# Performance work log

Measured on AMD Instinct MI355X. Metric: run time of the kernel, lower is better.

The kernel has to match this reference:

```python
import jax, jax.numpy as jnp
import numpy as np

D = 1024
H = 16
DH = D // H
F = 4096
B, S = 4, 2048
EPS = 1e-5


def _ln(x, g, b):
    m = jnp.mean(x, axis=-1, keepdims=True)
    v = jnp.var(x, axis=-1, keepdims=True)
    return (x - m) * jax.lax.rsqrt(v + EPS) * g + b


def setup_inputs() -> dict:
    key = jax.random.key(0)
    ks = jax.random.split(key, 16)
    s = 0.02
    return {
        "x": jax.random.normal(ks[0], (B, S, D), jnp.float32),
        "key_padding_mask": jnp.zeros((B, S), jnp.bool_),
        "Wq": jax.random.normal(ks[1], (D, D), jnp.float32) * s,
        "bq": jnp.zeros((D,), jnp.float32),
        "Wk": jax.random.normal(ks[2], (D, D), jnp.float32) * s,
        "bk": jnp.zeros((D,), jnp.float32),
        "Wv": jax.random.normal(ks[3], (D, D), jnp.float32) * s,
        "bv": jnp.zeros((D,), jnp.float32),
        "Wo": jax.random.normal(ks[4], (D, D), jnp.float32) * s,
        "bo": jnp.zeros((D,), jnp.float32),
        "W1": jax.random.normal(ks[5], (F, D), jnp.float32) * s,
        "b1": jnp.zeros((F,), jnp.float32),
        "W2": jax.random.normal(ks[6], (D, F), jnp.float32) * s,
        "b2": jnp.zeros((D,), jnp.float32),
        "ln1_g": jnp.ones((D,), jnp.float32),
        "ln1_b": jnp.zeros((D,), jnp.float32),
        "ln2_g": jnp.ones((D,), jnp.float32),
        "ln2_b": jnp.zeros((D,), jnp.float32),
    }


def _attn(x, kpm, Wq, bq, Wk, bk, Wv, bv, Wo, bo):
    b, s, d = x.shape
    scaling = DH ** (-0.5)
    q = (x @ Wq.T + bq) * scaling
    k = x @ Wk.T + bk
    v = x @ Wv.T + bv
    q = q.reshape(b, s, H, DH)
    k = k.reshape(b, s, H, DH)
    v = v.reshape(b, s, H, DH)
    # [b,h,q,k]
    scores = jnp.einsum("bqhd,bkhd->bhqk", q, k)
    scores = jnp.where(kpm[:, None, None, :], -jnp.inf, scores)
    p = jax.nn.softmax(scores.astype(jnp.float32), axis=-1).astype(q.dtype)
    out = jnp.einsum("bhqk,bkhd->bqhd", p, v).reshape(b, s, d)
    return out @ Wo.T + bo


def reference(x, key_padding_mask, Wq, bq, Wk, bk, Wv, bv, Wo, bo,
              W1, b1, W2, b2, ln1_g, ln1_b, ln2_g, ln2_b):
    # post-LN (normalize_before=False), dropout in eval mode (identity)
    x = _ln(x + _attn(x, key_padding_mask, Wq, bq, Wk, bk, Wv, bv, Wo, bo), ln1_g, ln1_b)
    h = jax.nn.gelu(x @ W1.T + b1, approximate=False)
    x = _ln(x + (h @ W2.T + b2), ln2_g, ln2_b)
    return x
```

## Files before the change

kernel.cpp:

```cpp
#include <hip/hip_runtime.h>
#include <hip/hip_bf16.h>
#include <math.h>

typedef short bf16x8 __attribute__((ext_vector_type(8)));
typedef float f32x4 __attribute__((ext_vector_type(4)));

__device__ __forceinline__ unsigned short f2bfu(float f) {
    __hip_bfloat16 h = __float2bfloat16(f);
    return __builtin_bit_cast(unsigned short, h);
}

__device__ __forceinline__ float fexp2(float x) {
    float r;
    asm("v_exp_f32 %0, %1" : "=v"(r) : "v"(x));
    return r;
}

__device__ __forceinline__ unsigned cvtpk_bf16(float lo, float hi) {
    unsigned r;
    asm("v_cvt_pk_bf16_f32 %0, %1, %2" : "=v"(r) : "v"(lo), "v"(hi));
    return r;
}

__device__ __forceinline__ float gelu_fast(float x) {
    const float x2 = x * x;
    const float z = x * (0.7978845608f + 0.0356774081f * x2);
    const float e = fexp2(z * 2.88539008f);
    const float r = __builtin_amdgcn_rcpf(e + 1.0f);
    return x * (1.0f - r);
}

__device__ __forceinline__ void gload_lds16(const void* gsrc, void* ldst) {
    __builtin_amdgcn_global_load_lds((const __attribute__((address_space(1))) void*)gsrc,
                                     (__attribute__((address_space(3))) void*)ldst,
                                     16, 0, 0);
}

#define MFMA __builtin_amdgcn_mfma_f32_16x16x32_bf16

__global__ __launch_bounds__(256)
void cvt_bf16_kernel(const float4* __restrict__ in, ushort4* __restrict__ out, int n4) {
    int i = blockIdx.x * 256 + threadIdx.x;
    if (i >= n4) return;
    float4 v = in[i];
    ushort4 o;
    o.x = f2bfu(v.x); o.y = f2bfu(v.y); o.z = f2bfu(v.z); o.w = f2bfu(v.w);
    out[i] = o;
}

enum { EPI_QKV = 0, EPI_RESF32 = 2, EPI_GELU = 3, EPI_RESBF16 = 5 };

template<int EPI>
__global__ __launch_bounds__(256, 3)
void gemm_bt(const __hip_bfloat16* __restrict__ A,
             const __hip_bfloat16* __restrict__ W,
             const float* __restrict__ bias,
             const void* __restrict__ resv,
             float scale,
             void* __restrict__ outp, void* __restrict__ outp2, void* __restrict__ outp3,
             int M, int N, int K)
{
    __shared__ __hip_bfloat16 As[3][128 * 32];
    __shared__ __hip_bfloat16 Ws[3][128 * 32];
    const int tid = threadIdx.x;
    const int lane = tid & 63;
    const int wid = tid >> 6;
    const int wr = wid >> 1, wc = wid & 1;
    const int g = lane >> 4, lr = lane & 15;
    const int row0 = blockIdx.x * 128;
    const int col0 = blockIdx.y * 128;

    f32x4 acc[4][4];
    const f32x4 zero = {0.f, 0.f, 0.f, 0.f};
#pragma unroll
    for (int m = 0; m < 4; ++m)
#pragma unroll
        for (int n = 0; n < 4; ++n) acc[m][n] = zero;

    const int c0 = tid, c1 = tid + 256;
    const int ar0 = c0 >> 2, ac0 = (c0 & 3) * 8;
    const int ar1 = c1 >> 2, ac1 = (c1 & 3) * 8;
    const __hip_bfloat16* Arow0 = A + (size_t)(row0 + ar0) * K + ac0;
    const __hip_bfloat16* Arow1 = A + (size_t)(row0 + ar1) * K + ac1;
    const __hip_bfloat16* Wrow0 = W + (size_t)(col0 + ar0) * K + ac0;
    const __hip_bfloat16* Wrow1 = W + (size_t)(col0 + ar1) * K + ac1;

    auto stage = [&](int bi, int k0) {
        gload_lds16(Arow0 + k0, (char*)As[bi] + c0 * 16);
        gload_lds16(Arow1 + k0, (char*)As[bi] + c1 * 16);
        gload_lds16(Wrow0 + k0, (char*)Ws[bi] + c0 * 16);
        gload_lds16(Wrow1 + k0, (char*)Ws[bi] + c1 * 16);
    };

    const int NT = K >> 5;
    stage(0, 0);
    stage(1, 32);
    asm volatile("s_waitcnt vmcnt(4)" ::: "memory");
    __builtin_amdgcn_s_barrier();
    __builtin_amdgcn_sched_barrier(0);

    int cur = 0, stg = 2;
    int kpre = 64;
    for (int t = 0; t < NT; ++t) {
        if (t + 2 < NT) stage(stg, kpre);

        bf16x8 af[4], wf[4];
#pragma unroll
        for (int m = 0; m < 4; ++m)
            af[m] = *(const bf16x8*)(As[cur] + (wr * 64 + m * 16 + lr) * 32 + g * 8);
#pragma unroll
        for (int n = 0; n < 4; ++n)
            wf[n] = *(const bf16x8*)(Ws[cur] + (wc * 64 + n * 16 + lr) * 32 + g * 8);
#pragma unroll
        for (int m = 0; m < 4; ++m)
#pragma unroll
            for (int n = 0; n < 4; ++n)
                acc[m][n] = MFMA(af[m], wf[n], acc[m][n], 0, 0, 0);

        if (t + 1 < NT) {
            if (t + 2 < NT) asm volatile("s_waitcnt vmcnt(4)" ::: "memory");
            else            asm volatile("s_waitcnt vmcnt(0)" ::: "memory");
            __builtin_amdgcn_s_barrier();
            __builtin_amdgcn_sched_barrier(0);
        }
        cur = (cur == 2) ? 0 : cur + 1;
        stg = (stg == 2) ? 0 : stg + 1;
        kpre += 32;
    }

#pragma unroll
    for (int n = 0; n < 4; ++n) {
        const int cc = col0 + wc * 64 + n * 16 + lr;
        const float bv = bias[cc];
#pragma unroll
        for (int m = 0; m < 4; ++m) {
            const int rbase = row0 + wr * 64 + m * 16 + g * 4;
            if (EPI == EPI_QKV) {
                const int seg = col0 >> 10;
                if (seg == 2) {
                    ushort4 u;
                    u.x = f2bfu(acc[m][n][0] + bv);
                    u.y = f2bfu(acc[m][n][1] + bv);
                    u.z = f2bfu(acc[m][n][2] + bv);
                    u.w = f2bfu(acc[m][n][3] + bv);
                    const int cc2 = cc - 2048;
                    const int h_ = cc2 >> 6, dh = cc2 & 63;
                    const int bb = rbase >> 11;
                    const int s = rbase & 2047;
                    *(ushort4*)((__hip_bfloat16*)outp3 +
                                (((size_t)bb * 16 + h_) * 64 + dh) * 2048 + s) = u;
                } else {
                    const float sc = (seg == 0) ? scale : 1.0f;
                    __hip_bfloat16* dst = (seg == 0) ? (__hip_bfloat16*)outp
                                                     : (__hip_bfloat16*)outp2;
                    const int ccl = cc & 1023;
#pragma unroll
                    for (int r = 0; r < 4; ++r)
                        dst[(size_t)(rbase + r) * 1024 + ccl] =
                            __float2bfloat16((acc[m][n][r] + bv) * sc);
                }
            } else {
#pragma unroll
                for (int r = 0; r < 4; ++r) {
                    const size_t idx = (size_t)(rbase + r) * N + cc;
                    float v = acc[m][n][r] + bv;
                    if (EPI == EPI_RESF32) {
                        ((float*)outp)[idx] = v + ((const float*)resv)[idx];
                    } else if (EPI == EPI_RESBF16) {
                        ((float*)outp)[idx] = v +
                            __bfloat162float(((const __hip_bfloat16*)resv)[idx]);
                    } else if (EPI == EPI_GELU) {
                        ((__hip_bfloat16*)outp)[idx] = __float2bfloat16(gelu_fast(v));
                    }
                }
            }
        }
    }
}

__global__ __launch_bounds__(256, 2)
void attn_flash2(const __hip_bfloat16* __restrict__ Q,
                 const __hip_bfloat16* __restrict__ K,
                 const __hip_bfloat16* __restrict__ VT,
                 const unsigned char* __restrict__ kpm,
                 __hip_bfloat16* __restrict__ O)
{
    __shared__ __hip_bfloat16 Ks[2][64 * 64];
    __shared__ __hip_bfloat16 VTs[2][64 * 64];
    __shared__ __hip_bfloat16 Plds[4][64 * 64];

    const int tid = threadIdx.x;
    const int lane = tid & 63;
    const int w = tid >> 6;
    const int g = lane >> 4, lr = lane & 15;

    const int orig = blockIdx.y * 8 + blockIdx.x;
    const int nl = (orig & 7) * 64 + (orig >> 3);
    const int qb = nl & 7;
    const int bh = nl >> 3;

    const int b = bh >> 4, h = bh & 15;
    const int q0 = qb * 256 + w * 64;
    const size_t tokbase = (size_t)b * 2048;
    const __hip_bfloat16* VTbh = VT + (size_t)bh * 64 * 2048;

    unsigned tmask = 0;
#pragma unroll
    for (int i = 0; i < 8; ++i) {
        const unsigned mv = *(const unsigned*)(kpm + tokbase + i * 256 + lane * 4);
        const unsigned long long bal = __ballot((int)(mv != 0u));
#pragma unroll
        for (int j = 0; j < 4; ++j)
            if ((bal >> (16 * j)) & 0xFFFFull) tmask |= (1u << (i * 4 + j));
    }

    bf16x8 qf[4][2];
#pragma unroll
    for (int qn = 0; qn < 4; ++qn)
#pragma unroll
        for (int f = 0; f < 2; ++f)
            qf[qn][f] = *(const bf16x8*)(Q + (tokbase + q0 + qn * 16 + lr) * 1024 +
                                         h * 64 + f * 32 + g * 8);

    f32x4 o[4][4];
    const f32x4 zero = {0.f, 0.f, 0.f, 0.f};
#pragma unroll
    for (int qa = 0; qa < 4; ++qa)
#pragma unroll
        for (int nd = 0; nd < 4; ++nd) o[qa][nd] = zero;
    float m_run[4], l_part[4];
#pragma unroll
    for (int qn = 0; qn < 4; ++qn) { m_run[qn] = -1e30f; l_part[qn] = 0.f; }

    __hip_bfloat16* Pw = Plds[w];
    const int rowl = lane >> 3;
    const int blkp = lane & 7;

    auto stage = [&](int bufi, int kv0) {
#pragma unroll
        for (int iss = 0; iss < 2; ++iss) {
            const int row = w * 16 + iss * 8 + rowl;
            const int sblk = blkp ^ (row & 7);
            gload_lds16(K + (tokbase + kv0 + row) * 1024 + h * 64 + sblk * 8,
                        (char*)&Ks[bufi][(w * 16 + iss * 8) * 64] + lane * 16);
            gload_lds16(VTbh + (size_t)row * 2048 + kv0 + sblk * 8,
                        (char*)&VTs[bufi][(w * 16 + iss * 8) * 64] + lane * 16);
        }
    };

    stage(0, 0);
    __syncthreads();
    int buf = 0;

    for (int t = 0; t < 32; ++t) {
        const int kv0 = t * 64;
        if (t < 31) stage(buf ^ 1, kv0 + 64);

        f32x4 st[4][4];
        __builtin_amdgcn_s_setprio(1);
#pragma unroll
        for (int km = 0; km < 4; ++km) {
            bf16x8 kf[2];
#pragma unroll
            for (int f = 0; f < 2; ++f)
                kf[f] = *(const bf16x8*)(&Ks[buf][(km * 16 + lr) * 64 +
                                                  (((f * 4 + g) ^ (lr & 7)) * 8)]);
#pragma unroll
            for (int qn = 0; qn < 4; ++qn) {
                st[km][qn] = MFMA(kf[0], qf[qn][0], zero, 0, 0, 0);
                st[km][qn] = MFMA(kf[1], qf[qn][1], st[km][qn], 0, 0, 0);
            }
        }
        __builtin_amdgcn_s_setprio(0);

        if (tmask & (1u << t)) {
            const float NEG = -1e30f;
#pragma unroll
            for (int km = 0; km < 4; ++km) {
                const unsigned mu = *(const unsigned*)(kpm + tokbase + kv0 + km * 16 + g * 4);
#pragma unroll
                for (int r = 0; r < 4; ++r) {
                    if ((mu >> (8 * r)) & 0xFFu) {
#pragma unroll
                        for (int qn = 0; qn < 4; ++qn) st[km][qn][r] = NEG;
                    }
                }
            }
        }

        float pm[4];
#pragma unroll
        for (int qn = 0; qn < 4; ++qn) {
            float a0 = fmaxf(fmaxf(st[0][qn][0], st[0][qn][1]), fmaxf(st[0][qn][2], st[0][qn][3]));
            float a1 = fmaxf(fmaxf(st[1][qn][0], st[1][qn][1]), fmaxf(st[1][qn][2], st[1][qn][3]));
            float a2 = fmaxf(fmaxf(st[2][qn][0], st[2][qn][1]), fmaxf(st[2][qn][2], st[2][qn][3]));
            float a3 = fmaxf(fmaxf(st[3][qn][0], st[3][qn][1]), fmaxf(st[3][qn][2], st[3][qn][3]));
            pm[qn] = fmaxf(fmaxf(a0, a1), fmaxf(a2, a3));
        }
        const int trig = (pm[0] > m_run[0] + 8.f) | (pm[1] > m_run[1] + 8.f) |
                         (pm[2] > m_run[2] + 8.f) | (pm[3] > m_run[3] + 8.f);
        if (__any(trig)) {
            float alpha_q[4];
#pragma unroll
            for (int qn = 0; qn < 4; ++qn) {
                float rm = pm[qn];
                rm = fmaxf(rm, __shfl_xor(rm, 16));
                rm = fmaxf(rm, __shfl_xor(rm, 32));
                const float mnew = fmaxf(m_run[qn], rm);
                const float al = fexp2(m_run[qn] - mnew);
                l_part[qn] *= al;
                m_run[qn] = mnew;
                alpha_q[qn] = al;
            }
#pragma unroll
            for (int qa = 0; qa < 4; ++qa)
#pragma unroll
                for (int r = 0; r < 4; ++r) {
                    const float av = __shfl(alpha_q[qa], g * 4 + r, 16);
#pragma unroll
                    for (int nd = 0; nd < 4; ++nd) o[qa][nd][r] *= av;
                }
        }

#pragma unroll
        for (int qn = 0; qn < 4; ++qn) {
            const float mm = m_run[qn];
#pragma unroll
            for (int km = 0; km < 4; ++km) {
                const float p0 = fexp2(st[km][qn][0] - mm);
                const float p1 = fexp2(st[km][qn][1] - mm);
                const float p2 = fexp2(st[km][qn][2] - mm);
                const float p3 = fexp2(st[km][qn][3] - mm);
                l_part[qn] += (p0 + p1) + (p2 + p3);
                uint2 pk;
                pk.x = cvtpk_bf16(p0, p1);
                pk.y = cvtpk_bf16(p2, p3);
                const int cs = (km * 2 + (g >> 1)) ^ (lr & 7);
                *(uint2*)(Pw + (qn * 16 + lr) * 64 + cs * 8 + (g & 1) * 4) = pk;
            }
        }

        __builtin_amdgcn_s_setprio(1);
#pragma unroll
        for (int f = 0; f < 2; ++f) {
            bf16x8 pa[4];
#pragma unroll
            for (int qa = 0; qa < 4; ++qa)
                pa[qa] = *(const bf16x8*)(Pw + (qa * 16 + lr) * 64 +
                                          (((f * 4 + g) ^ (lr & 7)) * 8));
#pragma unroll
            for (int nd = 0; nd < 4; ++nd) {
                bf16x8 vb = *(const bf16x8*)(&VTs[buf][(nd * 16 + lr) * 64 +
                                                       (((f * 4 + g) ^ (lr & 7)) * 8)]);
#pragma unroll
                for (int qa = 0; qa < 4; ++qa)
                    o[qa][nd] = MFMA(pa[qa], vb, o[qa][nd], 0, 0, 0);
            }
        }
        __builtin_amdgcn_s_setprio(0);

        __syncthreads();
        buf ^= 1;
    }

    float linv[4];
#pragma unroll
    for (int qn = 0; qn < 4; ++qn) {
        float lt = l_part[qn];
        lt += __shfl_xor(lt, 16);
        lt += __shfl_xor(lt, 32);
        linv[qn] = 1.0f / lt;
    }
#pragma unroll
    for (int qa = 0; qa < 4; ++qa)
#pragma unroll
        for (int r = 0; r < 4; ++r) {
            const float lv = __shfl(linv[qa], g * 4 + r, 16);
            const size_t row = tokbase + q0 + qa * 16 + g * 4 + r;
#pragma unroll
            for (int nd = 0; nd < 4; ++nd)
                O[row * 1024 + h * 64 + nd * 16 + lr] = __float2bfloat16(o[qa][nd][r] * lv);
        }
}

__global__ __launch_bounds__(256)
void ln_kernel(const float* __restrict__ in, const float* __restrict__ gamma,
               const float* __restrict__ beta, float* __restrict__ outf,
               __hip_bfloat16* __restrict__ outb)
{
    const int row = blockIdx.x;
    const int tid = threadIdx.x;
    float4 v = ((const float4*)(in + (size_t)row * 1024))[tid];
    float s = v.x + v.y + v.z + v.w;
    float s2 = v.x * v.x + v.y * v.y + v.z * v.z + v.w * v.w;
#pragma unroll
    for (int off = 1; off < 64; off <<= 1) {
        s += __shfl_xor(s, off);
        s2 += __shfl_xor(s2, off);
    }
    __shared__ float red[8];
    const int wv = tid >> 6;
    if ((tid & 63) == 0) { red[wv] = s; red[4 + wv] = s2; }
    __syncthreads();
    s = red[0] + red[1] + red[2] + red[3];
    s2 = red[4] + red[5] + red[6] + red[7];
    const float mean = s * (1.f / 1024.f);
    const float var = s2 * (1.f / 1024.f) - mean * mean;
    const float rstd = rsqrtf(var + 1e-5f);
    float4 gm = ((const float4*)gamma)[tid];
    float4 bt = ((const float4*)beta)[tid];
    float4 y;
    y.x = (v.x - mean) * rstd * gm.x + bt.x;
    y.y = (v.y - mean) * rstd * gm.y + bt.y;
    y.z = (v.z - mean) * rstd * gm.z + bt.z;
    y.w = (v.w - mean) * rstd * gm.w + bt.w;
    if (outf) ((float4*)(outf + (size_t)row * 1024))[tid] = y;
    if (outb) {
        ushort4 ub;
        ub.x = f2bfu(y.x); ub.y = f2bfu(y.y); ub.z = f2bfu(y.z); ub.w = f2bfu(y.w);
        ((ushort4*)outb)[row * 256 + tid] = ub;
    }
}

extern "C" void kernel_launch(void* const* d_in, const int* in_sizes, int n_in,
                              void* d_out, int out_size, void* d_ws, size_t ws_size,
                              hipStream_t stream)
{
    const float* x    = (const float*)d_in[0];
    const unsigned char* kpm = (const unsigned char*)d_in[1];
    const float* Wq = (const float*)d_in[2];
    const float* bq = (const float*)d_in[3];
    const float* Wk = (const float*)d_in[4];
    const float* bk = (const float*)d_in[5];
    const float* Wv = (const float*)d_in[6];
    const float* bv = (const float*)d_in[7];
    const float* Wo = (const float*)d_in[8];
    const float* bo = (const float*)d_in[9];
    const float* W1 = (const float*)d_in[10];
    const float* b1 = (const float*)d_in[11];
    const float* W2 = (const float*)d_in[12];
    const float* b2 = (const float*)d_in[13];
    const float* ln1g = (const float*)d_in[14];
    const float* ln1b = (const float*)d_in[15];
    const float* ln2g = (const float*)d_in[16];
    const float* ln2b = (const float*)d_in[17];
    float* out = (float*)d_out;

    char* ws = (char*)d_ws;
    const size_t SZ_ND2 = (size_t)8192 * 1024 * 2;
    size_t off = 0;
    __hip_bfloat16* xb  = (__hip_bfloat16*)(ws + off); off += SZ_ND2;
    __hip_bfloat16* wqb = (__hip_bfloat16*)(ws + off); off += (size_t)1024 * 1024 * 2;
    __hip_bfloat16* wkb = (__hip_bfloat16*)(ws + off); off += (size_t)1024 * 1024 * 2;
    __hip_bfloat16* wvb = (__hip_bfloat16*)(ws + off); off += (size_t)1024 * 1024 * 2;
    __hip_bfloat16* wob = (__hip_bfloat16*)(ws + off); off += (size_t)1024 * 1024 * 2;
    __hip_bfloat16* w1b = (__hip_bfloat16*)(ws + off); off += (size_t)4096 * 1024 * 2;
    __hip_bfloat16* w2b = (__hip_bfloat16*)(ws + off); off += (size_t)4096 * 1024 * 2;
    const size_t qkv0 = off;
    __hip_bfloat16* qbp = (__hip_bfloat16*)(ws + off); off += SZ_ND2;
    __hip_bfloat16* kbp = (__hip_bfloat16*)(ws + off); off += SZ_ND2;
    __hip_bfloat16* vtg = (__hip_bfloat16*)(ws + off); off += SZ_ND2;
    __hip_bfloat16* abp = (__hip_bfloat16*)(ws + off); off += SZ_ND2;
    __hip_bfloat16* hbp = (__hip_bfloat16*)(ws + qkv0);
    float* y1 = (float*)(ws + off); off += (size_t)8192 * 1024 * 4;
    __hip_bfloat16* x1b = (__hip_bfloat16*)(ws + off); off += SZ_ND2;
    float* y2 = y1;
    float* bqkv = (float*)(ws + off); off += 3072 * 4;

    auto cvt = [&](const float* src, void* dst, int n) {
        cvt_bf16_kernel<<<n / 1024, 256, 0, stream>>>((const float4*)src, (ushort4*)dst, n / 4);
    };
    cvt(x,  xb,  8192 * 1024);
    cvt(Wq, wqb, 1024 * 1024);
    cvt(Wk, wkb, 1024 * 1024);
    cvt(Wv, wvb, 1024 * 1024);
    cvt(Wo, wob, 1024 * 1024);
    cvt(W1, w1b, 4096 * 1024);
    cvt(W2, w2b, 4096 * 1024);
    hipMemcpyAsync(bqkv,        bq, 4096, hipMemcpyDeviceToDevice, stream);
    hipMemcpyAsync(bqkv + 1024, bk, 4096, hipMemcpyDeviceToDevice, stream);
    hipMemcpyAsync(bqkv + 2048, bv, 4096, hipMemcpyDeviceToDevice, stream);

    dim3 blk(256);
    const float qscale = 0.125f * 1.44269504088896f;

    gemm_bt<EPI_QKV><<<dim3(64, 24), blk, 0, stream>>>(
        xb, wqb, bqkv, nullptr, qscale, qbp, kbp, vtg, 8192, 3072, 1024);

    attn_flash2<<<dim3(8, 64), blk, 0, stream>>>(qbp, kbp, vtg, kpm, abp);

    gemm_bt<EPI_RESF32><<<dim3(64, 8), blk, 0, stream>>>(
        abp, wob, bo, x, 1.0f, y1, nullptr, nullptr, 8192, 1024, 1024);
    ln_kernel<<<8192, 256, 0, stream>>>(y1, ln1g, ln1b, nullptr, x1b);

    gemm_bt<EPI_GELU><<<dim3(64, 32), blk, 0, stream>>>(
        x1b, w1b, b1, nullptr, 1.0f, hbp, nullptr, nullptr, 8192, 4096, 1024);
    gemm_bt<EPI_RESBF16><<<dim3(64, 8), blk, 0, stream>>>(
        hbp, w2b, b2, x1b, 1.0f, y2, nullptr, nullptr, 8192, 1024, 4096);
    ln_kernel<<<8192, 256, 0, stream>>>(y2, ln2g, ln2b, out, nullptr);
}
```

Baseline: 439.6 us.

## Make GEMMs persistent with cross-tile prefetch and configurable buffer depth

The GEMM kernel becomes persistent. A fixed grid loops over output tiles and prefetches the first k-slices of the next tile while finishing the current one, hiding the prologue load latency between tiles. The number of LDS stages is now a template parameter: 3 for the QKV and FFN1 GEMMs, 4 with lower occupancy for the Wo and FFN2 GEMMs. The tile ordering is column-major over M tiles, and the deeper pipeline trades occupancy for latency hiding.

Measured after the change: 447.2 us. About the same (+1.7%).

```diff
diff --git a/kernel.cpp b/kernel.cpp
--- a/kernel.cpp
+++ b/kernel.cpp
@@ -50,131 +50,159 @@
 
 enum { EPI_QKV = 0, EPI_RESF32 = 2, EPI_GELU = 3, EPI_RESBF16 = 5 };
 
-template<int EPI>
-__global__ __launch_bounds__(256, 3)
-void gemm_bt(const __hip_bfloat16* __restrict__ A,
-             const __hip_bfloat16* __restrict__ W,
-             const float* __restrict__ bias,
-             const void* __restrict__ resv,
-             float scale,
-             void* __restrict__ outp, void* __restrict__ outp2, void* __restrict__ outp3,
-             int M, int N, int K)
+template<int EPI, int NBUF>
+__global__ __launch_bounds__(256, (NBUF == 3) ? 3 : 2)
+void gemm_p(const __hip_bfloat16* __restrict__ A,
+            const __hip_bfloat16* __restrict__ W,
+            const float* __restrict__ bias,
+            const void* __restrict__ resv,
+            float scale,
+            void* __restrict__ outp, void* __restrict__ outp2, void* __restrict__ outp3,
+            int M, int N, int K, int TT )
 {
-    __shared__ __hip_bfloat16 As[3][128 * 32];
-    __shared__ __hip_bfloat16 Ws[3][128 * 32];
+    __shared__ __hip_bfloat16 As[NBUF][128 * 32];
+    __shared__ __hip_bfloat16 Ws[NBUF][128 * 32];
     const int tid = threadIdx.x;
     const int lane = tid & 63;
     const int wid = tid >> 6;
     const int wr = wid >> 1, wc = wid & 1;
     const int g = lane >> 4, lr = lane & 15;
-    const int row0 = blockIdx.x * 128;
-    const int col0 = blockIdx.y * 128;
-
-    f32x4 acc[4][4];
-    const f32x4 zero = {0.f, 0.f, 0.f, 0.f};
-#pragma unroll
-    for (int m = 0; m < 4; ++m)
-#pragma unroll
-        for (int n = 0; n < 4; ++n) acc[m][n] = zero;
+    const int G = gridDim.x;
+    const int mt = M >> 7;
+    const int NT = K >> 5;
 
     const int c0 = tid, c1 = tid + 256;
     const int ar0 = c0 >> 2, ac0 = (c0 & 3) * 8;
     const int ar1 = c1 >> 2, ac1 = (c1 & 3) * 8;
-    const __hip_bfloat16* Arow0 = A + (size_t)(row0 + ar0) * K + ac0;
-    const __hip_bfloat16* Arow1 = A + (size_t)(row0 + ar1) * K + ac1;
-    const __hip_bfloat16* Wrow0 = W + (size_t)(col0 + ar0) * K + ac0;
-    const __hip_bfloat16* Wrow1 = W + (size_t)(col0 + ar1) * K + ac1;
-
-    auto stage = [&](int bi, int k0) {
-        gload_lds16(Arow0 + k0, (char*)As[bi] + c0 * 16);
-        gload_lds16(Arow1 + k0, (char*)As[bi] + c1 * 16);
-        gload_lds16(Wrow0 + k0, (char*)Ws[bi] + c0 * 16);
-        gload_lds16(Wrow1 + k0, (char*)Ws[bi] + c1 * 16);
+
+    struct P { const __hip_bfloat16 *a0, *a1, *w0, *w1; };
+    auto mk = [&](int tl) -> P {
+        const int bx = tl % mt, by = tl / mt;
+        const int r0 = bx * 128, cl0 = by * 128;
+        P p;
+        p.a0 = A + (size_t)(r0 + ar0) * K + ac0;
+        p.a1 = A + (size_t)(r0 + ar1) * K + ac1;
+        p.w0 = W + (size_t)(cl0 + ar0) * K + ac0;
+        p.w1 = W + (size_t)(cl0 + ar1) * K + ac1;
+        return p;
     };
-
-    const int NT = K >> 5;
-    stage(0, 0);
-    stage(1, 32);
-    asm volatile("s_waitcnt vmcnt(4)" ::: "memory");
+    auto stage = [&](int bi, const P& p, int k0) {
+        gload_lds16(p.a0 + k0, (char*)As[bi] + c0 * 16);
+        gload_lds16(p.a1 + k0, (char*)As[bi] + c1 * 16);
+        gload_lds16(p.w0 + k0, (char*)Ws[bi] + c0 * 16);
+        gload_lds16(p.w1 + k0, (char*)Ws[bi] + c1 * 16);
+    };
+
+    int tile = blockIdx.x;
+    P pc = mk(tile);
+    bool hasN = (tile + G < TT);
+    P pn = hasN ? mk(tile + G) : pc;
+
+#pragma unroll
+    for (int i = 0; i < NBUF - 1; ++i) stage(i, pc, i * 32);
+    if (NBUF == 3) asm volatile("s_waitcnt vmcnt(4)" ::: "memory");
+    else           asm volatile("s_waitcnt vmcnt(8)" ::: "memory");
     __builtin_amdgcn_s_barrier();
     __builtin_amdgcn_sched_barrier(0);
 
-    int cur = 0, stg = 2;
-    int kpre = 64;
-    for (int t = 0; t < NT; ++t) {
-        if (t + 2 < NT) stage(stg, kpre);
-
-        bf16x8 af[4], wf[4];
+    int cur = 0, stg = NBUF - 1;
+
+    for (;;) {
+        f32x4 acc[4][4];
+        const f32x4 zero = {0.f, 0.f, 0.f, 0.f};
 #pragma unroll
         for (int m = 0; m < 4; ++m)
-            af[m] = *(const bf16x8*)(As[cur] + (wr * 64 + m * 16 + lr) * 32 + g * 8);
-#pragma unroll
-        for (int n = 0; n < 4; ++n)
-            wf[n] = *(const bf16x8*)(Ws[cur] + (wc * 64 + n * 16 + lr) * 32 + g * 8);
-#pragma unroll
-        for (int m = 0; m < 4; ++m)
+#pragma unroll
+            for (int n = 0; n < 4; ++n) acc[m][n] = zero;
+
+        for (int t = 0; t < NT; ++t) {
+            const int ahead = t + NBUF - 1;
+            if (ahead < NT)  stage(stg, pc, ahead * 32);
+            else if (hasN)   stage(stg, pn, (ahead - NT) * 32);
+
+            bf16x8 af[4], wf[4];
+#pragma unroll
+            for (int m = 0; m < 4; ++m)
+                af[m] = *(const bf16x8*)(As[cur] + (wr * 64 + m * 16 + lr) * 32 + g * 8);
 #pragma unroll
             for (int n = 0; n < 4; ++n)
-                acc[m][n] = MFMA(af[m], wf[n], acc[m][n], 0, 0, 0);
-
-        if (t + 1 < NT) {
-            if (t + 2 < NT) asm volatile("s_waitcnt vmcnt(4)" ::: "memory");
-            else            asm volatile("s_waitcnt vmcnt(0)" ::: "memory");
+                wf[n] = *(const bf16x8*)(Ws[cur] + (wc * 64 + n * 16 + lr) * 32 + g * 8);
+#pragma unroll
+            for (int m = 0; m < 4; ++m)
+#pragma unroll
+                for (int n = 0; n < 4; ++n)
+                    acc[m][n] = MFMA(af[m], wf[n], acc[m][n], 0, 0, 0);
+
+            if (NBUF == 3) {
+                if (t + 2 < NT || hasN) asm volatile("s_waitcnt vmcnt(4)" ::: "memory");
+                else                    asm volatile("s_waitcnt vmcnt(0)" ::: "memory");
+            } else {
+                if (t + 3 < NT || hasN) asm volatile("s_waitcnt vmcnt(8)" ::: "memory");
+                else if (t + 2 < NT)    asm volatile("s_waitcnt vmcnt(4)" ::: "memory");
+                else                    asm volatile("s_waitcnt vmcnt(0)" ::: "memory");
+            }
             __builtin_amdgcn_s_barrier();
             __builtin_amdgcn_sched_barrier(0);
-        }
-        cur = (cur == 2) ? 0 : cur + 1;
-        stg = (stg == 2) ? 0 : stg + 1;
-        kpre += 32;
-    }
-
-#pragma unroll
-    for (int n = 0; n < 4; ++n) {
-        const int cc = col0 + wc * 64 + n * 16 + lr;
-        const float bv = bias[cc];
-#pragma unroll
-        for (int m = 0; m < 4; ++m) {
-            const int rbase = row0 + wr * 64 + m * 16 + g * 4;
-            if (EPI == EPI_QKV) {
-                const int seg = col0 >> 10;
-                if (seg == 2) {
-                    ushort4 u;
-                    u.x = f2bfu(acc[m][n][0] + bv);
-                    u.y = f2bfu(acc[m][n][1] + bv);
-                    u.z = f2bfu(acc[m][n][2] + bv);
-                    u.w = f2bfu(acc[m][n][3] + bv);
-                    const int cc2 = cc - 2048;
-                    const int h_ = cc2 >> 6, dh = cc2 & 63;
-                    const int bb = rbase >> 11;
-                    const int s = rbase & 2047;
-                    *(ushort4*)((__hip_bfloat16*)outp3 +
-                                (((size_t)bb * 16 + h_) * 64 + dh) * 2048 + s) = u;
+            cur = (cur + 1 == NBUF) ? 0 : cur + 1;
+            stg = (stg + 1 == NBUF) ? 0 : stg + 1;
+        }
+
+        const int bx = tile % mt, by = tile / mt;
+        const int row0 = bx * 128, col0 = by * 128;
+#pragma unroll
+        for (int n = 0; n < 4; ++n) {
+            const int cc = col0 + wc * 64 + n * 16 + lr;
+            const float bv = bias[cc];
+#pragma unroll
+            for (int m = 0; m < 4; ++m) {
+                const int rbase = row0 + wr * 64 + m * 16 + g * 4;
+                if (EPI == EPI_QKV) {
+                    const int seg = col0 >> 10;
+                    if (seg == 2) {
+                        ushort4 u;
+                        u.x = f2bfu(acc[m][n][0] + bv);
+                        u.y = f2bfu(acc[m][n][1] + bv);
+                        u.z = f2bfu(acc[m][n][2] + bv);
+                        u.w = f2bfu(acc[m][n][3] + bv);
+                        const int cc2 = cc - 2048;
+                        const int h_ = cc2 >> 6, dh = cc2 & 63;
+                        const int bb = rbase >> 11;
+                        const int s = rbase & 2047;
+                        *(ushort4*)((__hip_bfloat16*)outp3 +
+                                    (((size_t)bb * 16 + h_) * 64 + dh) * 2048 + s) = u;
+                    } else {
+                        const float sc = (seg == 0) ? scale : 1.0f;
+                        __hip_bfloat16* dst = (seg == 0) ? (__hip_bfloat16*)outp
+                                                         : (__hip_bfloat16*)outp2;
+                        const int ccl = cc & 1023;
+#pragma unroll
+                        for (int r = 0; r < 4; ++r)
+                            dst[(size_t)(rbase + r) * 1024 + ccl] =
+                                __float2bfloat16((acc[m][n][r] + bv) * sc);
+                    }
                 } else {
-                    const float sc = (seg == 0) ? scale : 1.0f;
-                    __hip_bfloat16* dst = (seg == 0) ? (__hip_bfloat16*)outp
-                                                     : (__hip_bfloat16*)outp2;
-                    const int ccl = cc & 1023;
-#pragma unroll
-                    for (int r = 0; r < 4; ++r)
-                        dst[(size_t)(rbase + r) * 1024 + ccl] =
-                            __float2bfloat16((acc[m][n][r] + bv) * sc);
-                }
-            } else {
-#pragma unroll
-                for (int r = 0; r < 4; ++r) {
-                    const size_t idx = (size_t)(rbase + r) * N + cc;
-                    float v = acc[m][n][r] + bv;
-                    if (EPI == EPI_RESF32) {
-                        ((float*)outp)[idx] = v + ((const float*)resv)[idx];
-                    } else if (EPI == EPI_RESBF16) {
-                        ((float*)outp)[idx] = v +
-                            __bfloat162float(((const __hip_bfloat16*)resv)[idx]);
-                    } else if (EPI == EPI_GELU) {
-                        ((__hip_bfloat16*)outp)[idx] = __float2bfloat16(gelu_fast(v));
+#pragma unroll
+                    for (int r = 0; r < 4; ++r) {
+                        const size_t idx = (size_t)(rbase + r) * N + cc;
+                        float v = acc[m][n][r] + bv;
+                        if (EPI == EPI_RESF32) {
+                            ((float*)outp)[idx] = v + ((const float*)resv)[idx];
+                        } else if (EPI == EPI_RESBF16) {
+                            ((float*)outp)[idx] = v +
+                                __bfloat162float(((const __hip_bfloat16*)resv)[idx]);
+                        } else if (EPI == EPI_GELU) {
+                            ((__hip_bfloat16*)outp)[idx] = __float2bfloat16(gelu_fast(v));
+                        }
                     }
                 }
             }
         }
+
+        if (!hasN) break;
+        tile += G;
+        pc = pn;
+        hasN = (tile + G < TT);
+        if (hasN) pn = mk(tile + G);
     }
 }
 
@@ -484,18 +512,18 @@
     dim3 blk(256);
     const float qscale = 0.125f * 1.44269504088896f;
 
-    gemm_bt<EPI_QKV><<<dim3(64, 24), blk, 0, stream>>>(
-        xb, wqb, bqkv, nullptr, qscale, qbp, kbp, vtg, 8192, 3072, 1024);
+    gemm_p<EPI_QKV, 3><<<768, blk, 0, stream>>>(
+        xb, wqb, bqkv, nullptr, qscale, qbp, kbp, vtg, 8192, 3072, 1024, 1536);
 
     attn_flash2<<<dim3(8, 64), blk, 0, stream>>>(qbp, kbp, vtg, kpm, abp);
 
-    gemm_bt<EPI_RESF32><<<dim3(64, 8), blk, 0, stream>>>(
-        abp, wob, bo, x, 1.0f, y1, nullptr, nullptr, 8192, 1024, 1024);
+    gemm_p<EPI_RESF32, 4><<<512, blk, 0, stream>>>(
+        abp, wob, bo, x, 1.0f, y1, nullptr, nullptr, 8192, 1024, 1024, 512);
     ln_kernel<<<8192, 256, 0, stream>>>(y1, ln1g, ln1b, nullptr, x1b);
 
-    gemm_bt<EPI_GELU><<<dim3(64, 32), blk, 0, stream>>>(
-        x1b, w1b, b1, nullptr, 1.0f, hbp, nullptr, nullptr, 8192, 4096, 1024);
-    gemm_bt<EPI_RESBF16><<<dim3(64, 8), blk, 0, stream>>>(
-        hbp, w2b, b2, x1b, 1.0f, y2, nullptr, nullptr, 8192, 1024, 4096);
+    gemm_p<EPI_GELU, 3><<<768, blk, 0, stream>>>(
+        x1b, w1b, b1, nullptr, 1.0f, hbp, nullptr, nullptr, 8192, 4096, 1024, 2048);
+    gemm_p<EPI_RESBF16, 4><<<512, blk, 0, stream>>>(
+        hbp, w2b, b2, x1b, 1.0f, y2, nullptr, nullptr, 8192, 1024, 4096, 512);
     ln_kernel<<<8192, 256, 0, stream>>>(y2, ln2g, ln2b, out, nullptr);
 }
```

## Use wider 128x256 GEMM tiles for QKV and FFN1 projections

Applied to the files above, without the earlier changes.

Adds a gemm_w kernel with a 128x256 output tile. Each of its 4 waves covers all 128 rows and a 64-column strip, accumulating 8x4 MFMA tiles, and it keeps the same triple-buffered global-to-LDS pipeline. The QKV and W1 GEMMs switch to it, halving the grid along N and raising arithmetic intensity per byte loaded into LDS. In exchange it uses more registers and LDS per block (launch bounds lowered to 2 blocks/CU) and launches fewer blocks, which may reduce occupancy and latency hiding. The old gemm_bt drops its now-unused QKV epilogue.

New measurement: 449.1 us. 2.2% more time.

```diff
diff --git a/kernel.cpp b/kernel.cpp
--- a/kernel.cpp
+++ b/kernel.cpp
@@ -49,6 +49,145 @@
 }
 
 enum { EPI_QKV = 0, EPI_RESF32 = 2, EPI_GELU = 3, EPI_RESBF16 = 5 };
+
+template<int EPI>
+__global__ __launch_bounds__(256, 2)
+void gemm_w(const __hip_bfloat16* __restrict__ A,
+            const __hip_bfloat16* __restrict__ W,
+            const float* __restrict__ bias,
+            const void* __restrict__ resv,
+            float scale,
+            void* __restrict__ outp, void* __restrict__ outp2, void* __restrict__ outp3,
+            int M, int N, int K)
+{
+    __shared__ __hip_bfloat16 As[3][128 * 32];
+    __shared__ __hip_bfloat16 Ws[3][256 * 32];
+    const int tid = threadIdx.x;
+    const int lane = tid & 63;
+    const int w = tid >> 6;
+    const int g = lane >> 4, lr = lane & 15;
+    const int row0 = blockIdx.x * 128;
+    const int col0 = blockIdx.y * 256;
+
+    f32x4 acc[8][4];
+    const f32x4 zero = {0.f, 0.f, 0.f, 0.f};
+#pragma unroll
+    for (int m = 0; m < 8; ++m)
+#pragma unroll
+        for (int n = 0; n < 4; ++n) acc[m][n] = zero;
+
+    const int ra0 = tid >> 2;
+    const int ra1 = (tid + 256) >> 2;
+    const int ka0 = (((tid) & 3) ^ ((ra0 >> 1) & 3)) * 8;
+    const int ka1 = (((tid) & 3) ^ ((ra1 >> 1) & 3)) * 8;
+    const int rw0 = ra0, rw1 = ra1;
+    const int rw2 = (tid + 512) >> 2;
+    const int rw3 = (tid + 768) >> 2;
+    const int kw2 = (((tid) & 3) ^ ((rw2 >> 1) & 3)) * 8;
+    const int kw3 = (((tid) & 3) ^ ((rw3 >> 1) & 3)) * 8;
+
+    const __hip_bfloat16* Aa0 = A + (size_t)(row0 + ra0) * K + ka0;
+    const __hip_bfloat16* Aa1 = A + (size_t)(row0 + ra1) * K + ka1;
+    const __hip_bfloat16* Ww0 = W + (size_t)(col0 + rw0) * K + ka0;
+    const __hip_bfloat16* Ww1 = W + (size_t)(col0 + rw1) * K + ka1;
+    const __hip_bfloat16* Ww2 = W + (size_t)(col0 + rw2) * K + kw2;
+    const __hip_bfloat16* Ww3 = W + (size_t)(col0 + rw3) * K + kw3;
+
+    auto stage = [&](int bi, int k0) {
+        gload_lds16(Aa0 + k0, (char*)As[bi] + tid * 16);
+        gload_lds16(Aa1 + k0, (char*)As[bi] + (tid + 256) * 16);
+        gload_lds16(Ww0 + k0, (char*)Ws[bi] + tid * 16);
+        gload_lds16(Ww1 + k0, (char*)Ws[bi] + (tid + 256) * 16);
+        gload_lds16(Ww2 + k0, (char*)Ws[bi] + (tid + 512) * 16);
+        gload_lds16(Ww3 + k0, (char*)Ws[bi] + (tid + 768) * 16);
+    };
+
+    const int NT = K >> 5;
+    stage(0, 0);
+    stage(1, 32);
+    asm volatile("s_waitcnt vmcnt(6)" ::: "memory");
+    __builtin_amdgcn_s_barrier();
+    __builtin_amdgcn_sched_barrier(0);
+
+    const int swl = (lr >> 1) & 3;
+    int cur = 0, stg = 2, kpre = 64;
+
+    for (int t = 0; t < NT; ++t) {
+        if (t + 2 < NT) stage(stg, kpre);
+
+        bf16x8 af[8], wf[4];
+#pragma unroll
+        for (int m = 0; m < 8; ++m)
+            af[m] = *(const bf16x8*)(As[cur] + (m * 16 + lr) * 32 + (g ^ swl) * 8);
+#pragma unroll
+        for (int n = 0; n < 4; ++n)
+            wf[n] = *(const bf16x8*)(Ws[cur] + (w * 64 + n * 16 + lr) * 32 + (g ^ swl) * 8);
+#pragma unroll
+        for (int m = 0; m < 8; ++m)
+#pragma unroll
+            for (int n = 0; n < 4; ++n)
+                acc[m][n] = MFMA(af[m], wf[n], acc[m][n], 0, 0, 0);
+
+        if (t + 1 < NT) {
+            if (t + 2 < NT) asm volatile("s_waitcnt vmcnt(6)" ::: "memory");
+            else            asm volatile("s_waitcnt vmcnt(0)" ::: "memory");
+            __builtin_amdgcn_s_barrier();
+            __builtin_amdgcn_sched_barrier(0);
+        }
+        cur = (cur == 2) ? 0 : cur + 1;
+        stg = (stg == 2) ? 0 : stg + 1;
+        kpre += 32;
+    }
+
+#pragma unroll
+    for (int n = 0; n < 4; ++n) {
+        const int cc = col0 + w * 64 + n * 16 + lr;
+        const float bv = bias[cc];
+#pragma unroll
+        for (int m = 0; m < 8; ++m) {
+            const int rbase = row0 + m * 16 + g * 4;
+            if (EPI == EPI_QKV) {
+                const int seg = col0 >> 10;
+                if (seg == 2) {
+                    ushort4 u;
+                    u.x = f2bfu(acc[m][n][0] + bv);
+                    u.y = f2bfu(acc[m][n][1] + bv);
+                    u.z = f2bfu(acc[m][n][2] + bv);
+                    u.w = f2bfu(acc[m][n][3] + bv);
+                    const int cc2 = cc - 2048;
+                    const int h_ = cc2 >> 6, dh = cc2 & 63;
+                    const int bb = rbase >> 11;
+                    const int s = rbase & 2047;
+                    *(ushort4*)((__hip_bfloat16*)outp3 +
+                                (((size_t)bb * 16 + h_) * 64 + dh) * 2048 + s) = u;
+                } else {
+                    const float sc = (seg == 0) ? scale : 1.0f;
+                    __hip_bfloat16* dst = (seg == 0) ? (__hip_bfloat16*)outp
+                                                     : (__hip_bfloat16*)outp2;
+                    const int ccl = cc & 1023;
+#pragma unroll
+                    for (int r = 0; r < 4; ++r)
+                        dst[(size_t)(rbase + r) * 1024 + ccl] =
+                            __float2bfloat16((acc[m][n][r] + bv) * sc);
+                }
+            } else {
+#pragma unroll
+                for (int r = 0; r < 4; ++r) {
+                    const size_t idx = (size_t)(rbase + r) * N + cc;
+                    float v = acc[m][n][r] + bv;
+                    if (EPI == EPI_RESF32) {
+                        ((float*)outp)[idx] = v + ((const float*)resv)[idx];
+                    } else if (EPI == EPI_RESBF16) {
+                        ((float*)outp)[idx] = v +
+                            __bfloat162float(((const __hip_bfloat16*)resv)[idx]);
+                    } else if (EPI == EPI_GELU) {
+                        ((__hip_bfloat16*)outp)[idx] = __float2bfloat16(gelu_fast(v));
+                    }
+                }
+            }
+        }
+    }
+}
 
 template<int EPI>
 __global__ __launch_bounds__(256, 3)
@@ -135,43 +274,17 @@
 #pragma unroll
         for (int m = 0; m < 4; ++m) {
             const int rbase = row0 + wr * 64 + m * 16 + g * 4;
-            if (EPI == EPI_QKV) {
-                const int seg = col0 >> 10;
-                if (seg == 2) {
-                    ushort4 u;
-                    u.x = f2bfu(acc[m][n][0] + bv);
-                    u.y = f2bfu(acc[m][n][1] + bv);
-                    u.z = f2bfu(acc[m][n][2] + bv);
-                    u.w = f2bfu(acc[m][n][3] + bv);
-                    const int cc2 = cc - 2048;
-                    const int h_ = cc2 >> 6, dh = cc2 & 63;
-                    const int bb = rbase >> 11;
-                    const int s = rbase & 2047;
-                    *(ushort4*)((__hip_bfloat16*)outp3 +
-                                (((size_t)bb * 16 + h_) * 64 + dh) * 2048 + s) = u;
-                } else {
-                    const float sc = (seg == 0) ? scale : 1.0f;
-                    __hip_bfloat16* dst = (seg == 0) ? (__hip_bfloat16*)outp
-                                                     : (__hip_bfloat16*)outp2;
-                    const int ccl = cc & 1023;
-#pragma unroll
-                    for (int r = 0; r < 4; ++r)
-                        dst[(size_t)(rbase + r) * 1024 + ccl] =
-                            __float2bfloat16((acc[m][n][r] + bv) * sc);
-                }
-            } else {
-#pragma unroll
-                for (int r = 0; r < 4; ++r) {
-                    const size_t idx = (size_t)(rbase + r) * N + cc;
-                    float v = acc[m][n][r] + bv;
-                    if (EPI == EPI_RESF32) {
-                        ((float*)outp)[idx] = v + ((const float*)resv)[idx];
-                    } else if (EPI == EPI_RESBF16) {
-                        ((float*)outp)[idx] = v +
-                            __bfloat162float(((const __hip_bfloat16*)resv)[idx]);
-                    } else if (EPI == EPI_GELU) {
-                        ((__hip_bfloat16*)outp)[idx] = __float2bfloat16(gelu_fast(v));
-                    }
+#pragma unroll
+            for (int r = 0; r < 4; ++r) {
+                const size_t idx = (size_t)(rbase + r) * N + cc;
+                float v = acc[m][n][r] + bv;
+                if (EPI == EPI_RESF32) {
+                    ((float*)outp)[idx] = v + ((const float*)resv)[idx];
+                } else if (EPI == EPI_RESBF16) {
+                    ((float*)outp)[idx] = v +
+                        __bfloat162float(((const __hip_bfloat16*)resv)[idx]);
+                } else if (EPI == EPI_GELU) {
+                    ((__hip_bfloat16*)outp)[idx] = __float2bfloat16(gelu_fast(v));
                 }
             }
         }
@@ -484,7 +597,7 @@
     dim3 blk(256);
     const float qscale = 0.125f * 1.44269504088896f;
 
-    gemm_bt<EPI_QKV><<<dim3(64, 24), blk, 0, stream>>>(
+    gemm_w<EPI_QKV><<<dim3(64, 12), blk, 0, stream>>>(
         xb, wqb, bqkv, nullptr, qscale, qbp, kbp, vtg, 8192, 3072, 1024);
 
     attn_flash2<<<dim3(8, 64), blk, 0, stream>>>(qbp, kbp, vtg, kpm, abp);
@@ -493,7 +606,7 @@
         abp, wob, bo, x, 1.0f, y1, nullptr, nullptr, 8192, 1024, 1024);
     ln_kernel<<<8192, 256, 0, stream>>>(y1, ln1g, ln1b, nullptr, x1b);
 
-    gemm_bt<EPI_GELU><<<dim3(64, 32), blk, 0, stream>>>(
+    gemm_w<EPI_GELU><<<dim3(64, 16), blk, 0, stream>>>(
         x1b, w1b, b1, nullptr, 1.0f, hbp, nullptr, nullptr, 8192, 4096, 1024);
     gemm_bt<EPI_RESBF16><<<dim3(64, 8), blk, 0, stream>>>(
         hbp, w2b, b2, x1b, 1.0f, y2, nullptr, nullptr, 8192, 1024, 4096);
```
